# Optimization experiments

Hardware: AMD Instinct MI355X
Metric: run time of the kernel (lower is better)

Reference implementation:

```python
import jax, jax.numpy as jnp
import numpy as np

N, E = 100000, 1600000
NFEAT, NHID, NCLASS, NLAYER = 128, 128, 40, 3


def _glorot(key, shape):
    fan_in, fan_out = shape[0], shape[1]
    lim = float(np.sqrt(6.0 / (fan_in + fan_out)))
    return jax.random.uniform(key, shape, jnp.float32, -lim, lim)


def setup_inputs() -> dict:
    key = jax.random.key(0)
    ks = jax.random.split(key, 12)
    x = jax.random.normal(ks[0], (N, NFEAT), jnp.float32)
    src = jax.random.randint(ks[1], (E,), 0, N, jnp.int32)
    dst = jax.random.randint(ks[2], (E,), 0, N, jnp.int32)
    W1 = _glorot(ks[3], (NFEAT, NHID)); b1 = jnp.zeros((NHID,), jnp.float32)
    W2 = _glorot(ks[4], (NHID, NHID)); b2 = jnp.zeros((NHID,), jnp.float32)
    Wg = jnp.stack([_glorot(ks[5 + l], (NHID, NHID)) for l in range(NLAYER)])  # [L,H,H]
    bg = jnp.zeros((NLAYER, NHID), jnp.float32)
    Wc = _glorot(ks[5 + NLAYER], (NHID, NCLASS)); bc = jnp.zeros((NCLASS,), jnp.float32)
    return {"x": x, "src": src, "dst": dst, "W1": W1, "b1": b1, "W2": W2,
            "b2": b2, "Wg": Wg, "bg": bg, "Wc": Wc, "bc": bc}


def _graph_conv(h, src, dst, W, b, out_norm, in_norm):
    # DGL GraphConv norm='both': scale by src out-deg^{-1/2}, sum-aggregate,
    # scale by dst in-deg^{-1/2}, then linear (in_feats == out_feats -> W after agg).
    h = h * out_norm[:, None]
    agg = jax.ops.segment_sum(h[src], dst, num_segments=N)
    return (agg * in_norm[:, None]) @ W + b


def reference(x, src, dst, W1, b1, W2, b2, Wg, bg, Wc, bc):
    ones = jnp.ones((E,), jnp.float32)
    out_deg = jnp.clip(jax.ops.segment_sum(ones, src, num_segments=N), 1.0)
    in_deg = jnp.clip(jax.ops.segment_sum(ones, dst, num_segments=N), 1.0)
    out_norm = jax.lax.rsqrt(out_deg)
    in_norm = jax.lax.rsqrt(in_deg)

    h = x @ W1 + b1            # feature1
    h = h @ W2 + b2            # feature2
    for l in range(NLAYER):    # stacked GraphConv + ReLU (dropout is identity in eval)
        h = _graph_conv(h, src, dst, Wg[l], bg[l], out_norm, in_norm)
        h = jax.nn.relu(h)
    return h @ Wc + bc         # classifier
```

## Files before the change

kernel.cpp:

```cpp
#include <hip/hip_runtime.h>
#include <hip/hip_fp16.h>
#include <cstdint>
#include <cstddef>

constexpr int NN  = 100000;
constexpr int EE  = 1600000;
constexpr int HID = 128;
constexpr int NBUK = (NN + 511) / 512;
constexpr int BLKE = 2048;
constexpr int NBE  = (EE + BLKE - 1) / BLKE;
constexpr int MH   = NBUK * NBE;
constexpr int NSC  = (MH + 1023) / 1024;

typedef float f32x4_t __attribute__((ext_vector_type(4)));
typedef short bf16x8_t __attribute__((ext_vector_type(8)));

static __device__ __forceinline__ short f2bf(float f) {
    union { float f; unsigned u; } x; x.f = f;
    unsigned r = x.u + 0x7FFF + ((x.u >> 16) & 1);
    return (short)(r >> 16);
}
static __device__ __forceinline__ float bf2f(short b) {
    union { unsigned u; float f; } x; x.u = ((unsigned)(unsigned short)b) << 16;
    return x.f;
}

__global__ __launch_bounds__(256) void bh_both_k(const int* __restrict__ src, const int* __restrict__ dst,
                                                 int* __restrict__ bh_d, int* __restrict__ bh_s) {
    __shared__ int hd[NBUK], hs[NBUK];
    int blk = blockIdx.x, t = threadIdx.x;
    for (int i = t; i < NBUK; i += 256) { hd[i] = 0; hs[i] = 0; }
    __syncthreads();
    int e0 = blk * BLKE, e1 = min(e0 + BLKE, EE);
    for (int e = e0 + t; e < e1; e += 256) {
        atomicAdd(&hd[dst[e] >> 9], 1);
        atomicAdd(&hs[src[e] >> 9], 1);
    }
    __syncthreads();
    for (int i = t; i < NBUK; i += 256) {
        bh_d[i * NBE + blk] = hd[i];
        bh_s[i * NBE + blk] = hs[i];
    }
}

__global__ __launch_bounds__(256) void scan_sum_k(const int* __restrict__ in, int* __restrict__ bsum, int n) {
    __shared__ int sc[256];
    int b = blockIdx.x, t = threadIdx.x;
    int base = b * 1024 + t * 4;
    int s = 0;
#pragma unroll
    for (int j = 0; j < 4; j++) { int idx = base + j; s += (idx < n) ? in[idx] : 0; }
    sc[t] = s; __syncthreads();
    for (int off = 128; off > 0; off >>= 1) {
        if (t < off) sc[t] += sc[t + off];
        __syncthreads();
    }
    if (t == 0) bsum[b] = sc[0];
}

__global__ void scan_top_k(const int* __restrict__ bsum, int* __restrict__ boff, int nb) {
    __shared__ int sc[256];
    int t = threadIdx.x;
    int v = (t < nb) ? bsum[t] : 0;
    sc[t] = v; __syncthreads();
    for (int off = 1; off < 256; off <<= 1) {
        int u = (t >= off) ? sc[t - off] : 0;
        __syncthreads();
        sc[t] += u;
        __syncthreads();
    }
    if (t < nb) boff[t] = sc[t] - v;
}

__global__ __launch_bounds__(256) void scan_chunk_k(const int* __restrict__ in, const int* __restrict__ boff,
                                                    int* __restrict__ out, int n) {
    __shared__ int sc[256];
    int b = blockIdx.x, t = threadIdx.x;
    int base = b * 1024 + t * 4;
    int c[4];
#pragma unroll
    for (int j = 0; j < 4; j++) { int idx = base + j; c[j] = (idx < n) ? in[idx] : 0; }
    int s = c[0] + c[1] + c[2] + c[3];
    sc[t] = s; __syncthreads();
    for (int off = 1; off < 256; off <<= 1) {
        int v = (t >= off) ? sc[t - off] : 0;
        __syncthreads();
        sc[t] += v;
        __syncthreads();
    }
    int excl = sc[t] - s + boff[b];
#pragma unroll
    for (int j = 0; j < 4; j++) {
        int idx = base + j;
        if (idx < n) out[idx] = excl;
        excl += c[j];
    }
}

__global__ __launch_bounds__(256) void scatter_both_k(const int* __restrict__ src, const int* __restrict__ dst,
                                                      const int* __restrict__ off_d, const int* __restrict__ off_s,
                                                      int2* __restrict__ pairs, int* __restrict__ ssorted) {
    __shared__ int cd[NBUK], cs[NBUK];
    int blk = blockIdx.x, t = threadIdx.x;
    for (int i = t; i < NBUK; i += 256) {
        cd[i] = off_d[i * NBE + blk];
        cs[i] = off_s[i * NBE + blk];
    }
    __syncthreads();
    int e0 = blk * BLKE, e1 = min(e0 + BLKE, EE);
    for (int e = e0 + t; e < e1; e += 256) {
        int d = dst[e], s = src[e];
        int pd = atomicAdd(&cd[d >> 9], 1);
        pairs[pd] = make_int2(d, s);
        int ps = atomicAdd(&cs[s >> 9], 1);
        ssorted[ps] = s;
    }
}

__global__ __launch_bounds__(256) void bucket_csr_k(const int2* __restrict__ pairs, const int* __restrict__ off_d,
                                                    int* __restrict__ rowptr, int* __restrict__ col,
                                                    float* __restrict__ inorm) {
    __shared__ int hist[512];
    __shared__ int excl[512];
    __shared__ int psum[256];
    int b = blockIdx.x, t = threadIdx.x;
    int base = off_d[b * NBE];
    int endv = (b == NBUK - 1) ? EE : off_d[(b + 1) * NBE];
    hist[t] = 0; hist[t + 256] = 0;
    __syncthreads();
    for (int i = base + t; i < endv; i += 256) atomicAdd(&hist[pairs[i].x & 511], 1);
    __syncthreads();
    int p0 = hist[2 * t], p1 = hist[2 * t + 1];
    int ps = p0 + p1;
    psum[t] = ps; __syncthreads();
    for (int off = 1; off < 256; off <<= 1) {
        int u = (t >= off) ? psum[t - off] : 0;
        __syncthreads();
        psum[t] += u;
        __syncthreads();
    }
    int pex = psum[t] - ps;
    excl[2 * t] = pex; excl[2 * t + 1] = pex + p0;
    __syncthreads();
    int n0 = b * 512;
#pragma unroll
    for (int j = 0; j < 2; j++) {
        int i = 2 * t + j, node = n0 + i;
        if (node < NN) {
            rowptr[node] = base + excl[i];
            int c = hist[i]; if (c < 1) c = 1;
            inorm[node] = rsqrtf((float)c);
        }
    }
    if (b == NBUK - 1 && t == 0) rowptr[NN] = EE;
    __syncthreads();
    for (int i = base + t; i < endv; i += 256) {
        int2 p = pairs[i];
        int pos = base + atomicAdd(&excl[p.x & 511], 1);
        col[pos] = p.y;
    }
}

__global__ __launch_bounds__(256) void bucket_ocnt_k(const int* __restrict__ ssorted, const int* __restrict__ off_s,
                                                     float* __restrict__ onorm) {
    __shared__ int hist[512];
    int b = blockIdx.x, t = threadIdx.x;
    int base = off_s[b * NBE];
    int endv = (b == NBUK - 1) ? EE : off_s[(b + 1) * NBE];
    hist[t] = 0; hist[t + 256] = 0;
    __syncthreads();
    for (int i = base + t; i < endv; i += 256) atomicAdd(&hist[ssorted[i] & 511], 1);
    __syncthreads();
#pragma unroll
    for (int j = 0; j < 2; j++) {
        int i = t + j * 256, node = b * 512 + i;
        if (node < NN) {
            int c = hist[i]; if (c < 1) c = 1;
            onorm[node] = rsqrtf((float)c);
        }
    }
}

__global__ __launch_bounds__(256) void w12_k(const float* __restrict__ W1, const float* __restrict__ W2,
                                             float* __restrict__ W12) {
    int idx = blockIdx.x * 256 + threadIdx.x;
    int i = idx >> 7, j = idx & 127;
    float a0 = 0.f, a1 = 0.f, a2 = 0.f, a3 = 0.f;
    for (int k = 0; k < 128; k += 4) {
        a0 = fmaf(W1[i * 128 + k],     W2[(k)     * 128 + j], a0);
        a1 = fmaf(W1[i * 128 + k + 1], W2[(k + 1) * 128 + j], a1);
        a2 = fmaf(W1[i * 128 + k + 2], W2[(k + 2) * 128 + j], a2);
        a3 = fmaf(W1[i * 128 + k + 3], W2[(k + 3) * 128 + j], a3);
    }
    W12[idx] = (a0 + a1) + (a2 + a3);
}

__global__ void b12_k(const float* __restrict__ b1, const float* __restrict__ W2,
                      const float* __restrict__ b2, float* __restrict__ b12) {
    int j = threadIdx.x;
    if (j < 128) {
        float acc = b2[j];
        for (int k = 0; k < 128; k++) acc = fmaf(b1[k], W2[k * 128 + j], acc);
        b12[j] = acc;
    }
}

__global__ __launch_bounds__(256) void agg_k(const float4* __restrict__ h16, const int* __restrict__ rowptr,
                                             const int* __restrict__ col, float4* __restrict__ out) {
    int w = (int)((blockIdx.x * 256 + threadIdx.x) >> 6);
    if (w >= NN) return;
    int lane = threadIdx.x & 63;
    int q   = lane >> 4;
    int l16 = lane & 15;
    int beg = rowptr[w], end = rowptr[w + 1];
    float acc[8];
#pragma unroll
    for (int j = 0; j < 8; j++) acc[j] = 0.f;

    union HU { float4 f4; __half2 h2[4]; };
    int i = beg + q;
    for (; i + 12 < end; i += 16) {
        int s0 = col[i], s1 = col[i + 4], s2 = col[i + 8], s3 = col[i + 12];
        HU u0, u1, u2, u3;
        u0.f4 = h16[(size_t)s0 * 16 + l16];
        u1.f4 = h16[(size_t)s1 * 16 + l16];
        u2.f4 = h16[(size_t)s2 * 16 + l16];
        u3.f4 = h16[(size_t)s3 * 16 + l16];
#pragma unroll
        for (int p = 0; p < 4; p++) {
            float2 a = __half22float2(u0.h2[p]);
            float2 b = __half22float2(u1.h2[p]);
            float2 c = __half22float2(u2.h2[p]);
            float2 d = __half22float2(u3.h2[p]);
            acc[2 * p]     += (a.x + b.x) + (c.x + d.x);
            acc[2 * p + 1] += (a.y + b.y) + (c.y + d.y);
        }
    }
    for (; i < end; i += 4) {
        int s = col[i];
        HU u; u.f4 = h16[(size_t)s * 16 + l16];
#pragma unroll
        for (int p = 0; p < 4; p++) {
            float2 a = __half22float2(u.h2[p]);
            acc[2 * p]     += a.x;
            acc[2 * p + 1] += a.y;
        }
    }
#pragma unroll
    for (int mm = 16; mm <= 32; mm <<= 1)
#pragma unroll
        for (int j = 0; j < 8; j++) acc[j] += __shfl_xor(acc[j], mm);
    if (q == 0) {
        float4 o0, o1;
        o0.x = acc[0]; o0.y = acc[1]; o0.z = acc[2]; o0.w = acc[3];
        o1.x = acc[4]; o1.y = acc[5]; o1.z = acc[6]; o1.w = acc[7];
        out[(size_t)w * 32 + l16 * 2]     = o0;
        out[(size_t)w * 32 + l16 * 2 + 1] = o1;
    }
}

template <int NT, bool RELU, bool INSCALE, bool OUTSCALE, bool OUTHALF>
__global__ __launch_bounds__(256) void mfma_gemm_k(
    const float* __restrict__ in, const float* __restrict__ inscale,
    const float* __restrict__ W, const float* __restrict__ bias,
    void* __restrict__ outp, const float* __restrict__ outscale,
    int nrows, int ncols, int ngroups) {

    __shared__ short Bh[NT * 2048];
    __shared__ short Bl[NT * 2048];

    const int t = threadIdx.x;

    if constexpr (NT == 8) {
        for (int j = 0; j < 16; j++) {
            int fi = (j * 256 + t) * 4;
            int k = fi >> 7, n0 = fi & 127;
            float4 wv = *(const float4*)(W + fi);
            float wa[4] = {wv.x, wv.y, wv.z, wv.w};
#pragma unroll
            for (int c = 0; c < 4; c++) {
                int n = n0 + c;
                int nt = n >> 4, kblk = k >> 5, ksub = k & 31;
                int lane_ = ((ksub >> 3) << 4) | (n & 15);
                int sidx = ((nt * 4 + kblk) * 64 + lane_) * 8 + (ksub & 7);
                short hi = f2bf(wa[c]);
                short lo = f2bf(wa[c] - bf2f(hi));
                Bh[sidx] = hi; Bl[sidx] = lo;
            }
        }
    } else {
        for (int idx = t; idx < 128 * 64; idx += 256) {
            int k = idx >> 6, n = idx & 63;
            if (n < NT * 16) {
                float w = (n < 40) ? W[k * 40 + n] : 0.f;
                int nt = n >> 4, kblk = k >> 5, ksub = k & 31;
                int lane_ = ((ksub >> 3) << 4) | (n & 15);
                int sidx = ((nt * 4 + kblk) * 64 + lane_) * 8 + (ksub & 7);
                short hi = f2bf(w);
                short lo = f2bf(w - bf2f(hi));
                Bh[sidx] = hi; Bl[sidx] = lo;
            }
        }
    }
    __syncthreads();

    const int wave = t >> 6;
    const int lane = t & 63;
    const int m    = lane & 15;
    const int kq   = lane >> 4;

    for (int g = blockIdx.x; g < ngroups; g += gridDim.x) {
        int grow0 = g * 64 + wave * 16;
        int row   = grow0 + m;
        bool rv   = row < nrows;

        bf16x8_t Ah[4], Al[4];
        float s = 1.f;
        if (INSCALE && rv) s = inscale[row];
#pragma unroll
        for (int kb = 0; kb < 4; kb++) {
            const float* ap = in + (size_t)row * 128 + kb * 32 + kq * 8;
            float4 p0, p1;
            if (rv) { p0 = *(const float4*)ap; p1 = *(const float4*)(ap + 4); }
            else    { p0 = make_float4(0,0,0,0); p1 = make_float4(0,0,0,0); }
            float av[8] = {p0.x, p0.y, p0.z, p0.w, p1.x, p1.y, p1.z, p1.w};
#pragma unroll
            for (int j = 0; j < 8; j++) {
                float v = INSCALE ? av[j] * s : av[j];
                short hi = f2bf(v);
                Ah[kb][j] = hi;
                Al[kb][j] = f2bf(v - bf2f(hi));
            }
        }

        int crow0 = grow0 + kq * 4;
        float osr[4];
#pragma unroll
        for (int r = 0; r < 4; r++) {
            int crow = crow0 + r;
            osr[r] = (OUTSCALE && crow < nrows) ? outscale[crow] : 1.f;
        }

#pragma unroll
        for (int nt = 0; nt < NT; nt++) {
            f32x4_t acc = {0.f, 0.f, 0.f, 0.f};
#pragma unroll
            for (int kb = 0; kb < 4; kb++) {
                const bf16x8_t bh = *(const bf16x8_t*)&Bh[((nt * 4 + kb) * 64 + lane) * 8];
                const bf16x8_t bl = *(const bf16x8_t*)&Bl[((nt * 4 + kb) * 64 + lane) * 8];
                acc = __builtin_amdgcn_mfma_f32_16x16x32_bf16(Ah[kb], bh, acc, 0, 0, 0);
                acc = __builtin_amdgcn_mfma_f32_16x16x32_bf16(Al[kb], bh, acc, 0, 0, 0);
                acc = __builtin_amdgcn_mfma_f32_16x16x32_bf16(Ah[kb], bl, acc, 0, 0, 0);
            }
            int ccol = nt * 16 + m;
            bool cv = (NT == 8) ? true : (ccol < ncols);
            float bv = cv ? bias[ccol] : 0.f;
#pragma unroll
            for (int r = 0; r < 4; r++) {
                int crow = crow0 + r;
                if (crow < nrows && cv) {
                    float v = acc[r] + bv;
                    if (RELU) v = fmaxf(v, 0.f);
                    v *= osr[r];
                    if (OUTHALF) ((__half*)outp)[(size_t)crow * ncols + ccol] = __float2half_rn(v);
                    else         ((float*)outp)[(size_t)crow * ncols + ccol] = v;
                }
            }
        }
    }
}

extern "C" void kernel_launch(void* const* d_in, const int* in_sizes, int n_in,
                              void* d_out, int out_size, void* d_ws, size_t ws_size,
                              hipStream_t stream) {
    const float* x   = (const float*)d_in[0];
    const int*   src = (const int*)d_in[1];
    const int*   dst = (const int*)d_in[2];
    const float* W1  = (const float*)d_in[3];
    const float* b1  = (const float*)d_in[4];
    const float* W2  = (const float*)d_in[5];
    const float* b2  = (const float*)d_in[6];
    const float* Wg  = (const float*)d_in[7];
    const float* bg  = (const float*)d_in[8];
    const float* Wc  = (const float*)d_in[9];
    const float* bc  = (const float*)d_in[10];
    float* out = (float*)d_out;

    char* ws = (char*)d_ws;
    size_t off = 0;
    auto alloc = [&](size_t bytes) -> void* {
        void* p = ws + off;
        off += (bytes + 255) & ~(size_t)255;
        return p;
    };
    float*  h0     = (float*)alloc((size_t)NN * HID * 4);
    float*  h1     = (float*)alloc((size_t)NN * HID * 4);
    __half* h16    = (__half*)alloc((size_t)NN * HID * 2);
    float*  W12    = (float*)alloc(128 * 128 * 4);
    float*  b12    = (float*)alloc(128 * 4);
    float*  onorm  = (float*)alloc((size_t)NN * 4);
    float*  inorm  = (float*)alloc((size_t)NN * 4);
    int*    rowptr = (int*)alloc((size_t)(NN + 1) * 4);
    int*    col    = (int*)alloc((size_t)EE * 4);
    int*    bh_d   = (int*)alloc((size_t)MH * 4);
    int*    bh_s   = (int*)alloc((size_t)MH * 4);
    int*    off_d  = (int*)alloc((size_t)MH * 4);
    int*    off_s  = (int*)alloc((size_t)MH * 4);
    int*    bsum   = (int*)alloc((size_t)NSC * 4);
    int*    boff   = (int*)alloc((size_t)NSC * 4);
    int2* pairs   = (int2*)h0;
    int*  ssorted = (int*)((char*)h0 + (size_t)EE * 8);

    bh_both_k<<<NBE, 256, 0, stream>>>(src, dst, bh_d, bh_s);
    scan_sum_k<<<NSC, 256, 0, stream>>>(bh_d, bsum, MH);
    scan_top_k<<<1, 256, 0, stream>>>(bsum, boff, NSC);
    scan_chunk_k<<<NSC, 256, 0, stream>>>(bh_d, boff, off_d, MH);
    scan_sum_k<<<NSC, 256, 0, stream>>>(bh_s, bsum, MH);
    scan_top_k<<<1, 256, 0, stream>>>(bsum, boff, NSC);
    scan_chunk_k<<<NSC, 256, 0, stream>>>(bh_s, boff, off_s, MH);
    scatter_both_k<<<NBE, 256, 0, stream>>>(src, dst, off_d, off_s, pairs, ssorted);
    bucket_csr_k<<<NBUK, 256, 0, stream>>>(pairs, off_d, rowptr, col, inorm);
    bucket_ocnt_k<<<NBUK, 256, 0, stream>>>(ssorted, off_s, onorm);

    w12_k<<<64, 256, 0, stream>>>(W1, W2, W12);
    b12_k<<<1, 128, 0, stream>>>(b1, W2, b2, b12);

    const int ngroups = (NN + 63) / 64;
    const int ggrid   = 512;

    mfma_gemm_k<8, false, false, true, true><<<ggrid, 256, 0, stream>>>(
        x, nullptr, W12, b12, h16, onorm, NN, 128, ngroups);
    for (int l = 0; l < 3; l++) {
        agg_k<<<(NN * 64 + 255) / 256, 256, 0, stream>>>(
            (const float4*)h16, rowptr, col, (float4*)h0);
        if (l < 2) {
            mfma_gemm_k<8, true, true, true, true><<<ggrid, 256, 0, stream>>>(
                h0, inorm, Wg + (size_t)l * 128 * 128, bg + (size_t)l * 128, h16, onorm, NN, 128, ngroups);
        } else {
            mfma_gemm_k<8, true, true, false, false><<<ggrid, 256, 0, stream>>>(
                h0, inorm, Wg + (size_t)l * 128 * 128, bg + (size_t)l * 128, h1, nullptr, NN, 128, ngroups);
        }
    }
    mfma_gemm_k<3, false, false, false, false><<<ggrid, 256, 0, stream>>>(
        h1, nullptr, Wc, bc, out, nullptr, NN, 40, ngroups);
}
```

Before: 584.6 us.

## Replace src-side bucket sort with global atomics and pack edge pairs into 32 bits

Out-degree is now counted with global atomics into an array instead of a second bucketed radix pass, which removes one scan chain, a scatter stream and a bucket kernel. Destination buckets shrink to 256 nodes, so each (dst, src) pair packs into one 32-bit word instead of an int2, halving pair traffic. The bias-fusion kernel is merged into the W12 kernel as an extra block. Nontemporal loads and stores are added in aggregation and GEMM input reads. Global atomics on random src indices may contend, and the top-level scan now needs more than 256 partial sums, hence 512 threads.

After: 624.6 us. 1.07x slower.

```diff
diff --git a/kernel.cpp b/kernel.cpp
--- a/kernel.cpp
+++ b/kernel.cpp
@@ -6,7 +6,8 @@
 constexpr int NN  = 100000;
 constexpr int EE  = 1600000;
 constexpr int HID = 128;
-constexpr int NBUK = (NN + 511) / 512;
+constexpr int BUK = 256;
+constexpr int NBUK = (NN + BUK - 1) / BUK;
 constexpr int BLKE = 2048;
 constexpr int NBE  = (EE + BLKE - 1) / BLKE;
 constexpr int MH   = NBUK * NBE;
@@ -25,21 +26,31 @@
     return x.f;
 }
 
-__global__ __launch_bounds__(256) void bh_both_k(const int* __restrict__ src, const int* __restrict__ dst,
-                                                 int* __restrict__ bh_d, int* __restrict__ bh_s) {
-    __shared__ int hd[NBUK], hs[NBUK];
+__global__ __launch_bounds__(256) void deg_zero_k(int* __restrict__ outdeg) {
+    int i = blockIdx.x * 256 + threadIdx.x;
+    if (i < NN) outdeg[i] = 0;
+}
+
+__global__ __launch_bounds__(256) void bh_d_k(const int* __restrict__ src, const int* __restrict__ dst,
+                                              int* __restrict__ bh_d, int* __restrict__ outdeg) {
+    __shared__ int hd[NBUK];
     int blk = blockIdx.x, t = threadIdx.x;
-    for (int i = t; i < NBUK; i += 256) { hd[i] = 0; hs[i] = 0; }
+    for (int i = t; i < NBUK; i += 256) hd[i] = 0;
     __syncthreads();
     int e0 = blk * BLKE, e1 = min(e0 + BLKE, EE);
     for (int e = e0 + t; e < e1; e += 256) {
-        atomicAdd(&hd[dst[e] >> 9], 1);
-        atomicAdd(&hs[src[e] >> 9], 1);
-    }
-    __syncthreads();
-    for (int i = t; i < NBUK; i += 256) {
-        bh_d[i * NBE + blk] = hd[i];
-        bh_s[i * NBE + blk] = hs[i];
+        atomicAdd(&hd[dst[e] >> 8], 1);
+        atomicAdd(&outdeg[src[e]], 1);
+    }
+    __syncthreads();
+    for (int i = t; i < NBUK; i += 256) bh_d[i * NBE + blk] = hd[i];
+}
+
+__global__ __launch_bounds__(256) void onorm_k(const int* __restrict__ outdeg, float* __restrict__ onorm) {
+    int i = blockIdx.x * 256 + threadIdx.x;
+    if (i < NN) {
+        int c = outdeg[i]; if (c < 1) c = 1;
+        onorm[i] = rsqrtf((float)c);
     }
 }
 
@@ -58,12 +69,12 @@
     if (t == 0) bsum[b] = sc[0];
 }
 
-__global__ void scan_top_k(const int* __restrict__ bsum, int* __restrict__ boff, int nb) {
-    __shared__ int sc[256];
+__global__ __launch_bounds__(512) void scan_top_k(const int* __restrict__ bsum, int* __restrict__ boff, int nb) {
+    __shared__ int sc[512];
     int t = threadIdx.x;
     int v = (t < nb) ? bsum[t] : 0;
     sc[t] = v; __syncthreads();
-    for (int off = 1; off < 256; off <<= 1) {
+    for (int off = 1; off < 512; off <<= 1) {
         int u = (t >= off) ? sc[t - off] : 0;
         __syncthreads();
         sc[t] += u;
@@ -97,92 +108,74 @@
     }
 }
 
-__global__ __launch_bounds__(256) void scatter_both_k(const int* __restrict__ src, const int* __restrict__ dst,
-                                                      const int* __restrict__ off_d, const int* __restrict__ off_s,
-                                                      int2* __restrict__ pairs, int* __restrict__ ssorted) {
-    __shared__ int cd[NBUK], cs[NBUK];
+__global__ __launch_bounds__(256) void scatter_d_k(const int* __restrict__ src, const int* __restrict__ dst,
+                                                   const int* __restrict__ off_d, unsigned* __restrict__ pairs) {
+    __shared__ int cd[NBUK];
     int blk = blockIdx.x, t = threadIdx.x;
-    for (int i = t; i < NBUK; i += 256) {
-        cd[i] = off_d[i * NBE + blk];
-        cs[i] = off_s[i * NBE + blk];
-    }
+    for (int i = t; i < NBUK; i += 256) cd[i] = off_d[i * NBE + blk];
     __syncthreads();
     int e0 = blk * BLKE, e1 = min(e0 + BLKE, EE);
     for (int e = e0 + t; e < e1; e += 256) {
         int d = dst[e], s = src[e];
-        int pd = atomicAdd(&cd[d >> 9], 1);
-        pairs[pd] = make_int2(d, s);
-        int ps = atomicAdd(&cs[s >> 9], 1);
-        ssorted[ps] = s;
-    }
-}
-
-__global__ __launch_bounds__(256) void bucket_csr_k(const int2* __restrict__ pairs, const int* __restrict__ off_d,
+        int pd = atomicAdd(&cd[d >> 8], 1);
+        pairs[pd] = ((unsigned)(d & 255) << 17) | (unsigned)s;
+    }
+}
+
+__global__ __launch_bounds__(512) void bucket_csr_k(const unsigned* __restrict__ pairs, const int* __restrict__ off_d,
                                                     int* __restrict__ rowptr, int* __restrict__ col,
                                                     float* __restrict__ inorm) {
-    __shared__ int hist[512];
-    __shared__ int excl[512];
-    __shared__ int psum[256];
+    __shared__ int hist[BUK];
+    __shared__ int excl[BUK];
+    __shared__ int psum[BUK];
     int b = blockIdx.x, t = threadIdx.x;
     int base = off_d[b * NBE];
     int endv = (b == NBUK - 1) ? EE : off_d[(b + 1) * NBE];
-    hist[t] = 0; hist[t + 256] = 0;
-    __syncthreads();
-    for (int i = base + t; i < endv; i += 256) atomicAdd(&hist[pairs[i].x & 511], 1);
-    __syncthreads();
-    int p0 = hist[2 * t], p1 = hist[2 * t + 1];
-    int ps = p0 + p1;
-    psum[t] = ps; __syncthreads();
-    for (int off = 1; off < 256; off <<= 1) {
-        int u = (t >= off) ? psum[t - off] : 0;
-        __syncthreads();
-        psum[t] += u;
-        __syncthreads();
-    }
-    int pex = psum[t] - ps;
-    excl[2 * t] = pex; excl[2 * t + 1] = pex + p0;
-    __syncthreads();
-    int n0 = b * 512;
-#pragma unroll
-    for (int j = 0; j < 2; j++) {
-        int i = 2 * t + j, node = n0 + i;
+    if (t < BUK) hist[t] = 0;
+    __syncthreads();
+    for (int i = base + t; i < endv; i += 512) atomicAdd(&hist[pairs[i] >> 17], 1);
+    __syncthreads();
+    int ps = 0;
+    if (t < BUK) { ps = hist[t]; psum[t] = ps; }
+    __syncthreads();
+    for (int off = 1; off < BUK; off <<= 1) {
+        int u = 0;
+        if (t < BUK && t >= off) u = psum[t - off];
+        __syncthreads();
+        if (t < BUK) psum[t] += u;
+        __syncthreads();
+    }
+    if (t < BUK) {
+        int pex = psum[t] - ps;
+        excl[t] = pex;
+        int node = b * BUK + t;
         if (node < NN) {
-            rowptr[node] = base + excl[i];
-            int c = hist[i]; if (c < 1) c = 1;
+            rowptr[node] = base + pex;
+            int c = ps; if (c < 1) c = 1;
             inorm[node] = rsqrtf((float)c);
         }
     }
     if (b == NBUK - 1 && t == 0) rowptr[NN] = EE;
     __syncthreads();
-    for (int i = base + t; i < endv; i += 256) {
-        int2 p = pairs[i];
-        int pos = base + atomicAdd(&excl[p.x & 511], 1);
-        col[pos] = p.y;
-    }
-}
-
-__global__ __launch_bounds__(256) void bucket_ocnt_k(const int* __restrict__ ssorted, const int* __restrict__ off_s,
-                                                     float* __restrict__ onorm) {
-    __shared__ int hist[512];
-    int b = blockIdx.x, t = threadIdx.x;
-    int base = off_s[b * NBE];
-    int endv = (b == NBUK - 1) ? EE : off_s[(b + 1) * NBE];
-    hist[t] = 0; hist[t + 256] = 0;
-    __syncthreads();
-    for (int i = base + t; i < endv; i += 256) atomicAdd(&hist[ssorted[i] & 511], 1);
-    __syncthreads();
-#pragma unroll
-    for (int j = 0; j < 2; j++) {
-        int i = t + j * 256, node = b * 512 + i;
-        if (node < NN) {
-            int c = hist[i]; if (c < 1) c = 1;
-            onorm[node] = rsqrtf((float)c);
-        }
+    for (int i = base + t; i < endv; i += 512) {
+        unsigned p = pairs[i];
+        int pos = base + atomicAdd(&excl[p >> 17], 1);
+        col[pos] = (int)(p & 0x1FFFFu);
     }
 }
 
 __global__ __launch_bounds__(256) void w12_k(const float* __restrict__ W1, const float* __restrict__ W2,
-                                             float* __restrict__ W12) {
+                                             const float* __restrict__ b1, const float* __restrict__ b2,
+                                             float* __restrict__ W12, float* __restrict__ b12) {
+    if (blockIdx.x == 64) {
+        int j = threadIdx.x;
+        if (j < 128) {
+            float acc = b2[j];
+            for (int k = 0; k < 128; k++) acc = fmaf(b1[k], W2[k * 128 + j], acc);
+            b12[j] = acc;
+        }
+        return;
+    }
     int idx = blockIdx.x * 256 + threadIdx.x;
     int i = idx >> 7, j = idx & 127;
     float a0 = 0.f, a1 = 0.f, a2 = 0.f, a3 = 0.f;
@@ -193,16 +186,6 @@
         a3 = fmaf(W1[i * 128 + k + 3], W2[(k + 3) * 128 + j], a3);
     }
     W12[idx] = (a0 + a1) + (a2 + a3);
-}
-
-__global__ void b12_k(const float* __restrict__ b1, const float* __restrict__ W2,
-                      const float* __restrict__ b2, float* __restrict__ b12) {
-    int j = threadIdx.x;
-    if (j < 128) {
-        float acc = b2[j];
-        for (int k = 0; k < 128; k++) acc = fmaf(b1[k], W2[k * 128 + j], acc);
-        b12[j] = acc;
-    }
 }
 
 __global__ __launch_bounds__(256) void agg_k(const float4* __restrict__ h16, const int* __restrict__ rowptr,
@@ -217,15 +200,19 @@
 #pragma unroll
     for (int j = 0; j < 8; j++) acc[j] = 0.f;
 
+    const char* hb = (const char*)h16 + (size_t)l16 * 16;
     union HU { float4 f4; __half2 h2[4]; };
     int i = beg + q;
     for (; i + 12 < end; i += 16) {
-        int s0 = col[i], s1 = col[i + 4], s2 = col[i + 8], s3 = col[i + 12];
+        int s0 = __builtin_nontemporal_load(col + i);
+        int s1 = __builtin_nontemporal_load(col + i + 4);
+        int s2 = __builtin_nontemporal_load(col + i + 8);
+        int s3 = __builtin_nontemporal_load(col + i + 12);
         HU u0, u1, u2, u3;
-        u0.f4 = h16[(size_t)s0 * 16 + l16];
-        u1.f4 = h16[(size_t)s1 * 16 + l16];
-        u2.f4 = h16[(size_t)s2 * 16 + l16];
-        u3.f4 = h16[(size_t)s3 * 16 + l16];
+        u0.f4 = *(const float4*)(hb + (unsigned)s0 * 256u);
+        u1.f4 = *(const float4*)(hb + (unsigned)s1 * 256u);
+        u2.f4 = *(const float4*)(hb + (unsigned)s2 * 256u);
+        u3.f4 = *(const float4*)(hb + (unsigned)s3 * 256u);
 #pragma unroll
         for (int p = 0; p < 4; p++) {
             float2 a = __half22float2(u0.h2[p]);
@@ -237,8 +224,8 @@
         }
     }
     for (; i < end; i += 4) {
-        int s = col[i];
-        HU u; u.f4 = h16[(size_t)s * 16 + l16];
+        int s = __builtin_nontemporal_load(col + i);
+        HU u; u.f4 = *(const float4*)(hb + (unsigned)s * 256u);
 #pragma unroll
         for (int p = 0; p < 4; p++) {
             float2 a = __half22float2(u.h2[p]);
@@ -251,11 +238,10 @@
 #pragma unroll
         for (int j = 0; j < 8; j++) acc[j] += __shfl_xor(acc[j], mm);
     if (q == 0) {
-        float4 o0, o1;
-        o0.x = acc[0]; o0.y = acc[1]; o0.z = acc[2]; o0.w = acc[3];
-        o1.x = acc[4]; o1.y = acc[5]; o1.z = acc[6]; o1.w = acc[7];
-        out[(size_t)w * 32 + l16 * 2]     = o0;
-        out[(size_t)w * 32 + l16 * 2 + 1] = o1;
+        f32x4_t o0 = {acc[0], acc[1], acc[2], acc[3]};
+        f32x4_t o1 = {acc[4], acc[5], acc[6], acc[7]};
+        __builtin_nontemporal_store(o0, (f32x4_t*)&out[(size_t)w * 32 + l16 * 2]);
+        __builtin_nontemporal_store(o1, (f32x4_t*)&out[(size_t)w * 32 + l16 * 2 + 1]);
     }
 }
 
@@ -320,9 +306,14 @@
 #pragma unroll
         for (int kb = 0; kb < 4; kb++) {
             const float* ap = in + (size_t)row * 128 + kb * 32 + kq * 8;
-            float4 p0, p1;
-            if (rv) { p0 = *(const float4*)ap; p1 = *(const float4*)(ap + 4); }
-            else    { p0 = make_float4(0,0,0,0); p1 = make_float4(0,0,0,0); }
+            f32x4_t p0, p1;
+            if (rv) {
+                p0 = __builtin_nontemporal_load((const f32x4_t*)ap);
+                p1 = __builtin_nontemporal_load((const f32x4_t*)(ap + 4));
+            } else {
+                p0 = (f32x4_t){0.f, 0.f, 0.f, 0.f};
+                p1 = (f32x4_t){0.f, 0.f, 0.f, 0.f};
+            }
             float av[8] = {p0.x, p0.y, p0.z, p0.w, p1.x, p1.y, p1.z, p1.w};
 #pragma unroll
             for (int j = 0; j < 8; j++) {
@@ -400,30 +391,25 @@
     float*  b12    = (float*)alloc(128 * 4);
     float*  onorm  = (float*)alloc((size_t)NN * 4);
     float*  inorm  = (float*)alloc((size_t)NN * 4);
+    int*    outdeg = (int*)alloc((size_t)NN * 4);
     int*    rowptr = (int*)alloc((size_t)(NN + 1) * 4);
     int*    col    = (int*)alloc((size_t)EE * 4);
     int*    bh_d   = (int*)alloc((size_t)MH * 4);
-    int*    bh_s   = (int*)alloc((size_t)MH * 4);
     int*    off_d  = (int*)alloc((size_t)MH * 4);
-    int*    off_s  = (int*)alloc((size_t)MH * 4);
     int*    bsum   = (int*)alloc((size_t)NSC * 4);
     int*    boff   = (int*)alloc((size_t)NSC * 4);
-    int2* pairs   = (int2*)h0;
-    int*  ssorted = (int*)((char*)h0 + (size_t)EE * 8);
-
-    bh_both_k<<<NBE, 256, 0, stream>>>(src, dst, bh_d, bh_s);
+    unsigned* pairs = (unsigned*)h0;
+
+    deg_zero_k<<<(NN + 255) / 256, 256, 0, stream>>>(outdeg);
+    bh_d_k<<<NBE, 256, 0, stream>>>(src, dst, bh_d, outdeg);
+    onorm_k<<<(NN + 255) / 256, 256, 0, stream>>>(outdeg, onorm);
     scan_sum_k<<<NSC, 256, 0, stream>>>(bh_d, bsum, MH);
-    scan_top_k<<<1, 256, 0, stream>>>(bsum, boff, NSC);
+    scan_top_k<<<1, 512, 0, stream>>>(bsum, boff, NSC);
     scan_chunk_k<<<NSC, 256, 0, stream>>>(bh_d, boff, off_d, MH);
-    scan_sum_k<<<NSC, 256, 0, stream>>>(bh_s, bsum, MH);
-    scan_top_k<<<1, 256, 0, stream>>>(bsum, boff, NSC);
-    scan_chunk_k<<<NSC, 256, 0, stream>>>(bh_s, boff, off_s, MH);
-    scatter_both_k<<<NBE, 256, 0, stream>>>(src, dst, off_d, off_s, pairs, ssorted);
-    bucket_csr_k<<<NBUK, 256, 0, stream>>>(pairs, off_d, rowptr, col, inorm);
-    bucket_ocnt_k<<<NBUK, 256, 0, stream>>>(ssorted, off_s, onorm);
-
-    w12_k<<<64, 256, 0, stream>>>(W1, W2, W12);
-    b12_k<<<1, 128, 0, stream>>>(b1, W2, b2, b12);
+    scatter_d_k<<<NBE, 256, 0, stream>>>(src, dst, off_d, pairs);
+    bucket_csr_k<<<NBUK, 512, 0, stream>>>(pairs, off_d, rowptr, col, inorm);
+
+    w12_k<<<65, 256, 0, stream>>>(W1, W2, b1, b2, W12, b12);
 
     const int ngroups = (NN + 63) / 64;
     const int ggrid   = 512;
```
